# Kernel tuning notes

Hardware: AMD Instinct MI355X
Metric: run time of the kernel (lower is better)

The kernel has to match this reference:

```python
import jax, jax.numpy as jnp
from jax import lax
import numpy as np

DIM, HEADS, WIN = 192, 8, 8
B, H, W = 4, 256, 256


def setup_inputs() -> dict:
    key = jax.random.key(0)
    ks = jax.random.split(key, 4)
    s = 0.02
    return {
        "x": jax.random.normal(ks[0], (B, DIM, H, W), jnp.float32),
        "temperature": jnp.ones((HEADS, 1, 1), jnp.float32),
        "qkv_w": jax.random.normal(ks[1], (3 * DIM, DIM, 1, 1), jnp.float32) * s,
        "qkv_b": jnp.zeros((3 * DIM,), jnp.float32),
        "dw_w": jax.random.normal(ks[2], (3 * DIM, 1, 3, 3), jnp.float32) * s,
        "dw_b": jnp.zeros((3 * DIM,), jnp.float32),
        "proj_w": jax.random.normal(ks[3], (DIM, DIM, 1, 1), jnp.float32) * s,
        "proj_b": jnp.zeros((DIM,), jnp.float32),
    }


def _conv(x, w, b, groups=1, pad='VALID'):
    y = lax.conv_general_dilated(x, w, (1, 1), pad,
                                 feature_group_count=groups,
                                 dimension_numbers=('NCHW', 'OIHW', 'NCHW'))
    return y + b[None, :, None, None]


def _l2norm(x, eps=1e-12):
    # F.normalize(dim=-1): x / max(||x||_2, eps)
    n = jnp.sqrt(jnp.sum(x * x, axis=-1, keepdims=True))
    return x / jnp.maximum(n, eps)


def _chan_attn(q, k, v, temp):
    # q,k,v: [n, heads, c_per_head, d]; channel-wise (CxC) attention
    q = _l2norm(q)
    k = _l2norm(k)
    attn = jnp.einsum('nhcd,nhed->nhce', q, k) * temp[None]
    attn = jax.nn.softmax(attn, axis=-1)
    return jnp.einsum('nhce,nhed->nhcd', attn, v)


def reference(x, temperature, qkv_w, qkv_b, dw_w, dw_b, proj_w, proj_b):
    b, c, h, w = x.shape
    win, heads = WIN, HEADS
    cph = c // heads

    qkv = _conv(x, qkv_w, qkv_b)
    qkv = _conv(qkv, dw_w, dw_b, groups=3 * c, pad='SAME')  # depthwise 3x3
    q, k, v = jnp.split(qkv, 3, axis=1)

    # ---- local (windowed) branch ----
    def win_part(t):
        t = t.reshape(b, c, h // win, win, w // win, win)
        t = t.transpose(0, 2, 4, 1, 3, 5)
        return t.reshape(-1, heads, cph, win * win)

    o1 = _chan_attn(win_part(q), win_part(k), win_part(v), temperature)
    o1 = o1.reshape(b, h // win, w // win, c, win, win)
    o1 = o1.transpose(0, 3, 1, 4, 2, 5).reshape(b, c, h, w)

    # ---- global branch ----
    def flat(t):
        return t.reshape(b, heads, cph, h * w)

    o2 = _chan_attn(flat(q), flat(k), flat(v), temperature)
    o2 = o2.reshape(b, c, h, w)

    return _conv(o1 + o2, proj_w, proj_b)
```

## Files before the change

kernel.cpp:

```cpp
#include <hip/hip_runtime.h>
#include <hip/hip_bf16.h>
#include <cstdint>
#include <cstddef>

#define HWPIX 65536
#define IMGW 256
#define CDIM 192
#define C3 576
#define NBATCH 4
#define NHEADS 8
#define CPH 24
#define KP 104

using bf16 = __hip_bfloat16;
typedef __attribute__((ext_vector_type(8))) short short8;
typedef __attribute__((ext_vector_type(4))) float f32x4;
typedef unsigned int u32;
typedef unsigned short u16;

__device__ __forceinline__ float b2f(bf16 v) { return __bfloat162float(v); }
__device__ __forceinline__ bf16 f2b(float v) { return __float2bfloat16(v); }
__device__ __forceinline__ float bu2f(u16 h) { return __uint_as_float((u32)h << 16); }
__device__ __forceinline__ u16 f2bu(float x) {
    bf16 h = __float2bfloat16(x);
    return *reinterpret_cast<u16*>(&h);
}
__device__ __forceinline__ u32 pack2(float a, float b) {
    return (u32)f2bu(a) | ((u32)f2bu(b) << 16);
}

__global__ __launch_bounds__(256) void prep_weights(
    const float* __restrict__ W, u16* __restrict__ Wb, int n)
{
    int i = blockIdx.x * 256 + threadIdx.x;
    if (i < n) Wb[i] = f2bu(W[i]);
}

__global__ __launch_bounds__(256) void xprep_kernel(
    const float* __restrict__ X, u16* __restrict__ Xt)
{
    __shared__ float sX[CDIM * 68];
    const int b  = blockIdx.y;
    const int p0 = blockIdx.x * 64;
    const int tid = threadIdx.x;

#pragma unroll
    for (int i = 0; i < 12; ++i) {
        const int idx = tid + i * 256;
        const int p4 = idx & 15, k = idx >> 4;
        const float4 v = *reinterpret_cast<const float4*>(
            X + ((size_t)b * CDIM + k) * HWPIX + p0 + p4 * 4);
        *reinterpret_cast<float4*>(&sX[k * 68 + p4 * 4]) = v;
    }
    __syncthreads();

    const int p = tid >> 2;
    const int seg = tid & 3;
    u16* dst = Xt + ((size_t)b * HWPIX + p0 + p) * CDIM;
#pragma unroll
    for (int s = 0; s < 6; ++s) {
        const int blk = seg * 6 + s;
        float f[8];
#pragma unroll
        for (int j = 0; j < 8; ++j) f[j] = sX[(blk * 8 + j) * 68 + p];
        uint4 ov;
        ov.x = pack2(f[0], f[1]);
        ov.y = pack2(f[2], f[3]);
        ov.z = pack2(f[4], f[5]);
        ov.w = pack2(f[6], f[7]);
        *reinterpret_cast<uint4*>(dst + blk * 8) = ov;
    }
}

__global__ __launch_bounds__(256, 4) void conv_qkv_mfma(
    const u16* __restrict__ Xt, const u16* __restrict__ Wb,
    const float* __restrict__ bias, bf16* __restrict__ Y)
{
    __shared__ alignas(16) u16 sA[64 * KP];
    __shared__ alignas(16) u16 sB[128 * KP];
    __shared__ float sBias[64];

    int lin = blockIdx.x;
    lin = (lin & 7) * (18432 / 8) + (lin >> 3);
    const int co_t = lin % 9;
    const int rest = lin / 9;
    const int p_t = rest & 511;
    const int b   = rest >> 9;
    const int co0 = co_t * 64;
    const int p0  = p_t * 128;

    const int tid  = threadIdx.x;
    const int wave = tid >> 6;
    const int lane = tid & 63;
    const int r  = lane & 15;
    const int hk = lane >> 4;

    if (tid < 64) sBias[tid] = bias[co0 + tid];

    f32x4 acc[4][2];
#pragma unroll
    for (int i = 0; i < 4; ++i)
#pragma unroll
        for (int j = 0; j < 2; ++j) acc[i][j] = (f32x4){0.f, 0.f, 0.f, 0.f};

#pragma unroll
    for (int c = 0; c < 2; ++c) {
        {
            int idx = tid;
#pragma unroll
            for (int i = 0; i < 3; ++i, idx += 256) {
                const int row = idx / 12, cv = idx % 12;
                const uint4 v = *reinterpret_cast<const uint4*>(
                    Wb + (size_t)(co0 + row) * CDIM + c * 96 + cv * 8);
                *reinterpret_cast<uint4*>(&sA[row * KP + cv * 8]) = v;
            }
        }
        {
            int idx = tid;
#pragma unroll
            for (int i = 0; i < 6; ++i, idx += 256) {
                const int row = idx / 12, cv = idx % 12;
                const uint4 v = *reinterpret_cast<const uint4*>(
                    Xt + ((size_t)b * HWPIX + p0 + row) * CDIM + c * 96 + cv * 8);
                *reinterpret_cast<uint4*>(&sB[row * KP + cv * 8]) = v;
            }
        }
        __syncthreads();

#pragma unroll
        for (int ks = 0; ks < 3; ++ks) {
            const int kof = ks * 32 + hk * 8;
            const u16* pA = &sA[r * KP + kof];
            const u16* pB = &sB[(wave * 32 + r) * KP + kof];
            const short8 a0 = *reinterpret_cast<const short8*>(pA);
            const short8 a1 = *reinterpret_cast<const short8*>(pA + 16 * KP);
            const short8 a2 = *reinterpret_cast<const short8*>(pA + 32 * KP);
            const short8 a3 = *reinterpret_cast<const short8*>(pA + 48 * KP);
            const short8 b0 = *reinterpret_cast<const short8*>(pB);
            const short8 b1 = *reinterpret_cast<const short8*>(pB + 16 * KP);
            acc[0][0] = __builtin_amdgcn_mfma_f32_16x16x32_bf16(a0, b0, acc[0][0], 0, 0, 0);
            acc[1][0] = __builtin_amdgcn_mfma_f32_16x16x32_bf16(a1, b0, acc[1][0], 0, 0, 0);
            acc[2][0] = __builtin_amdgcn_mfma_f32_16x16x32_bf16(a2, b0, acc[2][0], 0, 0, 0);
            acc[3][0] = __builtin_amdgcn_mfma_f32_16x16x32_bf16(a3, b0, acc[3][0], 0, 0, 0);
            acc[0][1] = __builtin_amdgcn_mfma_f32_16x16x32_bf16(a0, b1, acc[0][1], 0, 0, 0);
            acc[1][1] = __builtin_amdgcn_mfma_f32_16x16x32_bf16(a1, b1, acc[1][1], 0, 0, 0);
            acc[2][1] = __builtin_amdgcn_mfma_f32_16x16x32_bf16(a2, b1, acc[2][1], 0, 0, 0);
            acc[3][1] = __builtin_amdgcn_mfma_f32_16x16x32_bf16(a3, b1, acc[3][1], 0, 0, 0);
        }
        __syncthreads();
    }

    u16* sOut = sB;
#pragma unroll
    for (int mf = 0; mf < 4; ++mf) {
#pragma unroll
        for (int j = 0; j < 4; ++j) {
            const int row = mf * 16 + hk * 4 + j;
            const float bs = sBias[row];
            sOut[row * 128 + wave * 32 + r]      = f2bu(acc[mf][0][j] + bs);
            sOut[row * 128 + wave * 32 + r + 16] = f2bu(acc[mf][1][j] + bs);
        }
    }
    __syncthreads();
#pragma unroll
    for (int i = 0; i < 4; ++i) {
        const int idx = tid + i * 256;
        const int row = idx >> 4, cq = idx & 15;
        const uint4 v = *reinterpret_cast<const uint4*>(&sOut[row * 128 + cq * 8]);
        *reinterpret_cast<uint4*>(
            &Y[((size_t)b * C3 + co0 + row) * HWPIX + p0 + cq * 8]) = v;
    }
}

__global__ __launch_bounds__(256, 4) void conv_proj_mfma(
    const u16* __restrict__ X, const u16* __restrict__ Wb,
    const float* __restrict__ bias, float* __restrict__ Y)
{
    __shared__ alignas(16) u16 sA[64 * KP];
    __shared__ alignas(16) u16 sB[128 * KP];
    __shared__ float sBias[64];

    int lin = blockIdx.x;
    lin = (lin & 7) * (6144 / 8) + (lin >> 3);
    const int co_t = lin % 3;
    const int rest = lin / 3;
    const int p_t = rest & 511;
    const int b   = rest >> 9;
    const int co0 = co_t * 64;
    const int p0  = p_t * 128;

    const int tid  = threadIdx.x;
    const int wave = tid >> 6;
    const int lane = tid & 63;
    const int r  = lane & 15;
    const int hk = lane >> 4;

    if (tid < 64) sBias[tid] = bias[co0 + tid];

    f32x4 acc[4][2];
#pragma unroll
    for (int i = 0; i < 4; ++i)
#pragma unroll
        for (int j = 0; j < 2; ++j) acc[i][j] = (f32x4){0.f, 0.f, 0.f, 0.f};

    const int p4 = tid & 31;
    const int kq = tid >> 5;

#pragma unroll
    for (int c = 0; c < 2; ++c) {
        {
            int idx = tid;
#pragma unroll
            for (int i = 0; i < 3; ++i, idx += 256) {
                const int row = idx / 12, cv = idx % 12;
                const uint4 v = *reinterpret_cast<const uint4*>(
                    Wb + (size_t)(co0 + row) * CDIM + c * 96 + cv * 8);
                *reinterpret_cast<uint4*>(&sA[row * KP + cv * 8]) = v;
            }
        }
        {
            const u16* Xc = X + ((size_t)b * CDIM + c * 96) * HWPIX + p0;
#pragma unroll
            for (int i = 0; i < 6; ++i) {
                const int kp = kq + i * 8;
                const int k  = kp * 2;
                const uint2 va = *reinterpret_cast<const uint2*>(
                    Xc + (size_t)k * HWPIX + p4 * 4);
                const uint2 vb = *reinterpret_cast<const uint2*>(
                    Xc + (size_t)(k + 1) * HWPIX + p4 * 4);
                const int col = (((kp >> 2) ^ (p4 & 3)) << 3) | (k & 7);
                const u32 w0 = (va.x & 0xffffu) | (vb.x << 16);
                const u32 w1 = (va.x >> 16)     | (vb.x & 0xffff0000u);
                const u32 w2 = (va.y & 0xffffu) | (vb.y << 16);
                const u32 w3 = (va.y >> 16)     | (vb.y & 0xffff0000u);
                const int rb = p4 * 4;
                *reinterpret_cast<u32*>(&sB[(rb    ) * KP + col]) = w0;
                *reinterpret_cast<u32*>(&sB[(rb + 1) * KP + col]) = w1;
                *reinterpret_cast<u32*>(&sB[(rb + 2) * KP + col]) = w2;
                *reinterpret_cast<u32*>(&sB[(rb + 3) * KP + col]) = w3;
            }
        }
        __syncthreads();

#pragma unroll
        for (int ks = 0; ks < 3; ++ks) {
            const int kof = ks * 32 + hk * 8;
            const u16* pA = &sA[r * KP + kof];
            const int rowb = wave * 32 + r;
            const int colr = (((kof >> 3) ^ ((rowb >> 2) & 3)) << 3);
            const u16* pB = &sB[rowb * KP + colr];
            const short8 a0 = *reinterpret_cast<const short8*>(pA);
            const short8 a1 = *reinterpret_cast<const short8*>(pA + 16 * KP);
            const short8 a2 = *reinterpret_cast<const short8*>(pA + 32 * KP);
            const short8 a3 = *reinterpret_cast<const short8*>(pA + 48 * KP);
            const short8 b0 = *reinterpret_cast<const short8*>(pB);
            const short8 b1 = *reinterpret_cast<const short8*>(pB + 16 * KP);
            acc[0][0] = __builtin_amdgcn_mfma_f32_16x16x32_bf16(a0, b0, acc[0][0], 0, 0, 0);
            acc[1][0] = __builtin_amdgcn_mfma_f32_16x16x32_bf16(a1, b0, acc[1][0], 0, 0, 0);
            acc[2][0] = __builtin_amdgcn_mfma_f32_16x16x32_bf16(a2, b0, acc[2][0], 0, 0, 0);
            acc[3][0] = __builtin_amdgcn_mfma_f32_16x16x32_bf16(a3, b0, acc[3][0], 0, 0, 0);
            acc[0][1] = __builtin_amdgcn_mfma_f32_16x16x32_bf16(a0, b1, acc[0][1], 0, 0, 0);
            acc[1][1] = __builtin_amdgcn_mfma_f32_16x16x32_bf16(a1, b1, acc[1][1], 0, 0, 0);
            acc[2][1] = __builtin_amdgcn_mfma_f32_16x16x32_bf16(a2, b1, acc[2][1], 0, 0, 0);
            acc[3][1] = __builtin_amdgcn_mfma_f32_16x16x32_bf16(a3, b1, acc[3][1], 0, 0, 0);
        }
        __syncthreads();
    }

#pragma unroll
    for (int mf = 0; mf < 4; ++mf) {
#pragma unroll
        for (int j = 0; j < 4; ++j) {
            const int co = co0 + mf * 16 + hk * 4 + j;
            const float bs = sBias[mf * 16 + hk * 4 + j];
            const size_t base = ((size_t)b * CDIM + co) * HWPIX + p0 + wave * 32 + r;
            Y[base]      = acc[mf][0][j] + bs;
            Y[base + 16] = acc[mf][1][j] + bs;
        }
    }
}

__global__ __launch_bounds__(256) void dwconv_kernel(
    const bf16* __restrict__ In, const float* __restrict__ Wd,
    const float* __restrict__ bd, bf16* __restrict__ Out)
{
    __shared__ alignas(16) u16 sIn[10 * 256];
    const int bc = blockIdx.y;
    const int c = bc % C3;
    const size_t base = (size_t)bc * HWPIX;
    const int r0 = blockIdx.x * 8;
    const int tid = threadIdx.x;

    for (int idx = tid; idx < 320; idx += 256) {
        const int lr = idx >> 5, ch = idx & 31;
        const int gr = r0 + lr - 1;
        uint4 v = {0u, 0u, 0u, 0u};
        if ((unsigned)gr < IMGW)
            v = *reinterpret_cast<const uint4*>(&In[base + (size_t)gr * IMGW + ch * 8]);
        *reinterpret_cast<uint4*>(&sIn[lr * 256 + ch * 8]) = v;
    }
    __syncthreads();

    float wg[9];
#pragma unroll
    for (int t = 0; t < 9; ++t) wg[t] = Wd[c * 9 + t];

    const int rr = tid >> 5;
    const int px0 = (tid & 31) * 8;
    const float bias = bd[c];
    float acc[8];
#pragma unroll
    for (int j = 0; j < 8; ++j) acc[j] = bias;

#pragma unroll
    for (int dy = 0; dy < 3; ++dy) {
        const int row = rr + dy;
        const u16* rp = &sIn[row * 256];
        const short8 mv = *reinterpret_cast<const short8*>(&rp[px0]);
        float m[8];
#pragma unroll
        for (int j = 0; j < 8; ++j) m[j] = bu2f((u16)mv[j]);
        const float lft = (px0 > 0) ? bu2f(rp[px0 - 1]) : 0.f;
        const float rgt = (px0 + 8 < 256) ? bu2f(rp[px0 + 8]) : 0.f;
        const float w0 = wg[dy * 3], w1 = wg[dy * 3 + 1], w2 = wg[dy * 3 + 2];

        acc[0] = fmaf(w0, lft, acc[0]);
        acc[0] = fmaf(w1, m[0], acc[0]);
        acc[0] = fmaf(w2, m[1], acc[0]);
#pragma unroll
        for (int j = 1; j < 7; ++j) {
            acc[j] = fmaf(w0, m[j - 1], acc[j]);
            acc[j] = fmaf(w1, m[j], acc[j]);
            acc[j] = fmaf(w2, m[j + 1], acc[j]);
        }
        acc[7] = fmaf(w0, m[6], acc[7]);
        acc[7] = fmaf(w1, m[7], acc[7]);
        acc[7] = fmaf(w2, rgt, acc[7]);
    }

    uint4 ov;
    ov.x = pack2(acc[0], acc[1]);
    ov.y = pack2(acc[2], acc[3]);
    ov.z = pack2(acc[4], acc[5]);
    ov.w = pack2(acc[6], acc[7]);
    *reinterpret_cast<uint4*>(&Out[base + (size_t)(r0 + rr) * IMGW + px0]) = ov;
}

#define CS 328
#define PS 40
#define OS 36

__global__ __launch_bounds__(256, 3) void local_attn_kernel(
    const bf16* __restrict__ QKV, const float* __restrict__ temp,
    const float* __restrict__ Ag, u16* __restrict__ Osum)
{
    __shared__ alignas(16) u16 sMem[3 * 24 * CS];
    __shared__ float snq[4 * 32], snk[4 * 32];
    __shared__ float sAg[576];
    u16* const sQ = sMem;
    u16* const sK = sMem + 24 * CS;
    u16* const sV = sMem + 48 * CS;
    u16* const sP = sQ;
    u16* const sO = sK;

    const int wy    = blockIdx.x >> 3;
    const int strip = blockIdx.x & 7;
    const int head  = blockIdx.y;
    const int b     = blockIdx.z;
    const int x0    = strip * 32;
    const int tid   = threadIdx.x;
    const int w     = tid >> 6;
    const int lane  = tid & 63;
    const int r     = lane & 15;
    const int hk    = lane >> 4;

    {
        const float* Asrc = Ag + ((size_t)(b * NHEADS + head)) * 576;
        for (int idx = tid; idx < 576; idx += 256) sAg[idx] = Asrc[idx];
    }

#pragma unroll
    for (int i = 0; i < 9; ++i) {
        const int idx = tid + i * 256;
        const int tensor = idx / 768;
        const int rem = idx - tensor * 768;
        const int c  = rem >> 5;
        const int rw = (rem >> 2) & 7;
        const int ch = rem & 3;
        const size_t g = ((size_t)b * C3 + tensor * CDIM + head * CPH + c) * HWPIX
                       + (size_t)(wy * 8 + rw) * IMGW + x0 + ch * 8;
        const uint4 v = *reinterpret_cast<const uint4*>(&QKV[g]);
        u16* dst = sMem + tensor * (24 * CS);
        *reinterpret_cast<uint4*>(&dst[c * CS + rw * 40 + ch * 8]) = v;
    }
    __syncthreads();

    if (tid < 192) {
        const int qk = tid / 96;
        const int rem = tid - qk * 96;
        const int ww = rem / 24, c = rem % 24;
        const u16* sT = qk ? sK : sQ;
        const int off = c * CS + ww * 8;
        float s = 0.f;
#pragma unroll
        for (int rw = 0; rw < 8; ++rw) {
            const int rw2 = (rw + c) & 7;
            const short8 v = *reinterpret_cast<const short8*>(&sT[off + rw2 * 40]);
#pragma unroll
            for (int j = 0; j < 8; ++j) {
                const float f = bu2f((u16)v[j]);
                s = fmaf(f, f, s);
            }
        }
        const float inv = 1.f / fmaxf(sqrtf(s), 1e-12f);
        if (qk) snk[ww * 32 + c] = inv; else snq[ww * 32 + c] = inv;
    }
    __syncthreads();

    f32x4 accg[2][2];
#pragma unroll
    for (int i = 0; i < 2; ++i)
#pragma unroll
        for (int j = 0; j < 2; ++j) accg[i][j] = (f32x4){0.f, 0.f, 0.f, 0.f};

#pragma unroll
    for (int kk = 0; kk < 2; ++kk) {
        const int colA = (kk * 4 + hk) * 40 + w * 8;
        const short8 aq0 = *reinterpret_cast<const short8*>(&sQ[(r     ) * CS + colA]);
        const short8 aq1 = *reinterpret_cast<const short8*>(&sQ[(16 + r) * CS + colA]);
        const short8 bk0 = *reinterpret_cast<const short8*>(&sK[(r     ) * CS + colA]);
        const short8 bk1 = *reinterpret_cast<const short8*>(&sK[(16 + r) * CS + colA]);
        accg[0][0] = __builtin_amdgcn_mfma_f32_16x16x32_bf16(aq0, bk0, accg[0][0], 0, 0, 0);
        accg[0][1] = __builtin_amdgcn_mfma_f32_16x16x32_bf16(aq0, bk1, accg[0][1], 0, 0, 0);
        accg[1][0] = __builtin_amdgcn_mfma_f32_16x16x32_bf16(aq1, bk0, accg[1][0], 0, 0, 0);
        accg[1][1] = __builtin_amdgcn_mfma_f32_16x16x32_bf16(aq1, bk1, accg[1][1], 0, 0, 0);
    }
    __syncthreads();

    const float t = temp[head];
    const int e0 = lane & 15;
    const bool v1 = e0 < 8;
    const float ink0 = snk[w * 32 + e0];
    const float ink1 = snk[w * 32 + 16 + e0];

#pragma unroll
    for (int ct = 0; ct < 2; ++ct) {
#pragma unroll
        for (int j = 0; j < 4; ++j) {
            const int cidx = ct * 16 + hk * 4 + j;
            const float inq = snq[w * 32 + (cidx < CPH ? cidx : 0)];
            const float g0 = accg[ct][0][j] * inq * ink0 * t;
            const float g1 = v1 ? accg[ct][1][j] * inq * ink1 * t : -1e30f;
            float m = fmaxf(g0, g1);
#pragma unroll
            for (int mk = 8; mk >= 1; mk >>= 1) m = fmaxf(m, __shfl_xor(m, mk));
            const float p0 = __expf(g0 - m);
            const float p1 = v1 ? __expf(g1 - m) : 0.f;
            float s = p0 + p1;
#pragma unroll
            for (int mk = 8; mk >= 1; mk >>= 1) s += __shfl_xor(s, mk);
            const float inv = 1.f / s;
            if (cidx < CPH) {
                sP[w * 32 * PS + cidx * PS + e0] = f2bu(p0 * inv + sAg[cidx * CPH + e0]);
                if (v1) sP[w * 32 * PS + cidx * PS + 16 + e0]
                    = f2bu(p1 * inv + sAg[cidx * CPH + 16 + e0]);
            }
        }
    }
    __syncthreads();

    f32x4 acco[2][4];
#pragma unroll
    for (int i = 0; i < 2; ++i)
#pragma unroll
        for (int j = 0; j < 4; ++j) acco[i][j] = (f32x4){0.f, 0.f, 0.f, 0.f};

    short8 afr[2];
#pragma unroll
    for (int ct = 0; ct < 2; ++ct) {
        if (hk < 3)
            afr[ct] = *reinterpret_cast<const short8*>(
                &sP[w * 32 * PS + (ct * 16 + r) * PS + hk * 8]);
        else
            afr[ct] = (short8){0, 0, 0, 0, 0, 0, 0, 0};
    }
#pragma unroll
    for (int nt = 0; nt < 4; ++nt) {
        const int px = nt * 16 + r;
        const int colV = (px >> 3) * 40 + w * 8 + (px & 7);
        short8 bfr;
        if (hk < 3) {
#pragma unroll
            for (int j = 0; j < 8; ++j)
                bfr[j] = (short)sV[(hk * 8 + j) * CS + colV];
        } else {
            bfr = (short8){0, 0, 0, 0, 0, 0, 0, 0};
        }
        acco[0][nt] = __builtin_amdgcn_mfma_f32_16x16x32_bf16(afr[0], bfr, acco[0][nt], 0, 0, 0);
        acco[1][nt] = __builtin_amdgcn_mfma_f32_16x16x32_bf16(afr[1], bfr, acco[1][nt], 0, 0, 0);
    }

#pragma unroll
    for (int ct = 0; ct < 2; ++ct) {
#pragma unroll
        for (int j = 0; j < 4; ++j) {
            const int cidx = ct * 16 + hk * 4 + j;
            if (cidx >= CPH) continue;
#pragma unroll
            for (int nt = 0; nt < 4; ++nt) {
                const int px = nt * 16 + r;
                const int rpx = px >> 3, pxl = px & 7;
                sO[(rpx * 24 + cidx) * OS + w * 8 + pxl] = f2bu(acco[ct][nt][j]);
            }
        }
    }
    __syncthreads();

#pragma unroll
    for (int i = 0; i < 3; ++i) {
        const int idx = tid + i * 256;
        const int q4 = idx & 3;
        const int row = idx >> 2;
        const int c = row % 24, rw = row / 24;
        const u16* src = &sO[row * OS + q4 * 8];
        const uint2 lo = *reinterpret_cast<const uint2*>(src);
        const uint2 hi = *reinterpret_cast<const uint2*>(src + 4);
        uint4 v = {lo.x, lo.y, hi.x, hi.y};
        *reinterpret_cast<uint4*>(
            &Osum[((size_t)b * CDIM + head * CPH + c) * HWPIX
                  + (size_t)(wy * 8 + rw) * IMGW + x0 + q4 * 8]) = v;
    }
}

#define GRS 520

__global__ __launch_bounds__(256) void gstats_kernel(
    const bf16* __restrict__ QKV, float* __restrict__ Gp)
{
    __shared__ alignas(16) u16 sq[32 * GRS];
    __shared__ alignas(16) u16 sk[32 * GRS];

    const int chunk = blockIdx.x;
    const int bh = blockIdx.y;
    const int b = bh >> 3, head = bh & 7;
    const int tid = threadIdx.x;
    const int w = tid >> 6, lane = tid & 63;
    const int r = lane & 15, hk = lane >> 4;

    const size_t qb = ((size_t)b * C3 + head * CPH) * HWPIX;
    const size_t kb = qb + (size_t)CDIM * HWPIX;

    for (int idx = tid; idx < 1040; idx += 256) {
        const int t = idx >= 520;
        const int o = idx - t * 520;
        u16* d = (t ? sk : sq) + 24 * GRS + o * 8;
        *reinterpret_cast<uint4*>(d) = (uint4){0u, 0u, 0u, 0u};
    }

    f32x4 acc[2][2];
#pragma unroll
    for (int i = 0; i < 2; ++i)
#pragma unroll
        for (int j = 0; j < 2; ++j) acc[i][j] = (f32x4){0.f, 0.f, 0.f, 0.f};
    float nacc = 0.f;
    const int nrow = tid >> 2;
    const int nq4  = tid & 3;

    for (int st = 0; st < 8; ++st) {
        const int d0 = chunk * 4096 + st * 512;
        __syncthreads();
#pragma unroll
        for (int i = 0; i < 12; ++i) {
            const int idx = tid + i * 256;
            const int t = idx >= 1536;
            const int rem = idx - t * 1536;
            const int c = rem >> 6, dv = rem & 63;
            const uint4 v = *reinterpret_cast<const uint4*>(
                &QKV[(t ? kb : qb) + (size_t)c * HWPIX + d0 + dv * 8]);
            u16* dst = (t ? sk : sq) + c * GRS + dv * 8;
            *reinterpret_cast<uint4*>(dst) = v;
        }
        __syncthreads();

#pragma unroll
        for (int ks = 0; ks < 4; ++ks) {
            const int kof = w * 128 + ks * 32 + hk * 8;
            const short8 aq0 = *reinterpret_cast<const short8*>(&sq[(r     ) * GRS + kof]);
            const short8 aq1 = *reinterpret_cast<const short8*>(&sq[(16 + r) * GRS + kof]);
            const short8 bk0 = *reinterpret_cast<const short8*>(&sk[(r     ) * GRS + kof]);
            const short8 bk1 = *reinterpret_cast<const short8*>(&sk[(16 + r) * GRS + kof]);
            acc[0][0] = __builtin_amdgcn_mfma_f32_16x16x32_bf16(aq0, bk0, acc[0][0], 0, 0, 0);
            acc[0][1] = __builtin_amdgcn_mfma_f32_16x16x32_bf16(aq0, bk1, acc[0][1], 0, 0, 0);
            acc[1][0] = __builtin_amdgcn_mfma_f32_16x16x32_bf16(aq1, bk0, acc[1][0], 0, 0, 0);
            acc[1][1] = __builtin_amdgcn_mfma_f32_16x16x32_bf16(aq1, bk1, acc[1][1], 0, 0, 0);
        }

        if (nrow < 48) {
            const u16* rp = (nrow < 24 ? &sq[nrow * GRS] : &sk[(nrow - 24) * GRS]) + nq4 * 128;
#pragma unroll
            for (int i = 0; i < 16; ++i) {
                const short8 v = *reinterpret_cast<const short8*>(&rp[i * 8]);
#pragma unroll
                for (int j = 0; j < 8; ++j) {
                    const float f = bu2f((u16)v[j]);
                    nacc = fmaf(f, f, nacc);
                }
            }
        }
    }
    __syncthreads();

    float* red = reinterpret_cast<float*>(sq);
#pragma unroll
    for (int ct = 0; ct < 2; ++ct) {
#pragma unroll
        for (int et = 0; et < 2; ++et) {
#pragma unroll
            for (int j = 0; j < 4; ++j) {
                const int c = ct * 16 + hk * 4 + j;
                const int e = et * 16 + r;
                if (c < CPH && e < CPH)
                    red[(w * 24 + c) * 25 + e] = acc[ct][et][j];
            }
        }
    }
    __syncthreads();

    float* dst = Gp + ((size_t)bh * 32 + chunk) * 624;
    for (int idx = tid; idx < 576; idx += 256) {
        const int c = idx / 24, e = idx % 24;
        const int o = c * 25 + e;
        dst[idx] = red[o] + red[600 + o] + red[1200 + o] + red[1800 + o];
    }

    float ns = nacc;
    ns += __shfl_xor(ns, 1);
    ns += __shfl_xor(ns, 2);
    if (nrow < 48 && nq4 == 0) {
        if (nrow < 24) dst[576 + nrow] = ns;
        else           dst[600 + (nrow - 24)] = ns;
    }
}

__global__ __launch_bounds__(64) void gsoftmax_kernel(
    const float* __restrict__ Gp, const float* __restrict__ temp,
    float* __restrict__ A)
{
    __shared__ float red[624];
    const int bh = blockIdx.x, head = bh & 7;
    const int tid = threadIdx.x;

    for (int jj = tid; jj < 624; jj += 64) {
        float s = 0.f;
        for (int ch = 0; ch < 16; ++ch) s += Gp[((size_t)bh * 32 + ch) * 624 + jj];
        red[jj] = s;
    }
    __syncthreads();

    if (tid < CPH) {
        const int c = tid;
        const float t = temp[head];
        const float inq = 1.f / fmaxf(sqrtf(red[576 + c]), 1e-12f);
        float l[CPH]; float m = -1e30f;
        for (int e = 0; e < CPH; ++e) {
            const float ink = 1.f / fmaxf(sqrtf(red[600 + e]), 1e-12f);
            l[e] = red[c * CPH + e] * inq * ink * t;
            m = fmaxf(m, l[e]);
        }
        float s = 0.f;
        for (int e = 0; e < CPH; ++e) { l[e] = expf(l[e] - m); s += l[e]; }
        const float inv = 1.f / s;
        for (int e = 0; e < CPH; ++e) A[(size_t)bh * 576 + c * CPH + e] = l[e] * inv;
    }
}

extern "C" void kernel_launch(void* const* d_in, const int* in_sizes, int n_in,
                              void* d_out, int out_size, void* d_ws, size_t ws_size,
                              hipStream_t stream) {
    const float* x           = (const float*)d_in[0];
    const float* temperature = (const float*)d_in[1];
    const float* qkv_w       = (const float*)d_in[2];
    const float* qkv_b       = (const float*)d_in[3];
    const float* dw_w        = (const float*)d_in[4];
    const float* dw_b        = (const float*)d_in[5];
    const float* proj_w      = (const float*)d_in[6];
    const float* proj_b      = (const float*)d_in[7];
    float* out = (float*)d_out;

    char* ws = (char*)d_ws;
    constexpr size_t QKV_ELEMS = (size_t)NBATCH * C3 * HWPIX;
    constexpr size_t QKV_BYTES = QKV_ELEMS * sizeof(bf16);

    bf16* qkv1 = (bf16*)ws;
    bf16* qkv2 = (bf16*)(ws + QKV_BYTES);
    u16*  osum = (u16*)ws;
    float* Gp   = (float*)(ws + 2 * QKV_BYTES);
    float* Amat = Gp + (size_t)32 * 32 * 624;
    u16*  Wb    = (u16*)Gp;
    u16*  Wpb   = (u16*)(Amat + 32 * 576);
    u16*  Xt    = (u16*)qkv2;

    prep_weights<<<(C3 * CDIM + 255) / 256, 256, 0, stream>>>(qkv_w, Wb, C3 * CDIM);
    prep_weights<<<(CDIM * CDIM + 255) / 256, 256, 0, stream>>>(proj_w, Wpb, CDIM * CDIM);

    xprep_kernel<<<dim3(HWPIX / 64, NBATCH), 256, 0, stream>>>(x, Xt);

    conv_qkv_mfma<<<9 * 512 * NBATCH, 256, 0, stream>>>(Xt, Wb, qkv_b, qkv1);

    dwconv_kernel<<<dim3(32, NBATCH * C3), 256, 0, stream>>>(
        qkv1, dw_w, dw_b, qkv2);

    gstats_kernel<<<dim3(16, 32), 256, 0, stream>>>(qkv2, Gp);

    gsoftmax_kernel<<<32, 64, 0, stream>>>(Gp, temperature, Amat);

    local_attn_kernel<<<dim3(256, NHEADS, NBATCH), 256, 0, stream>>>(
        qkv2, temperature, Amat, osum);

    conv_proj_mfma<<<3 * 512 * NBATCH, 256, 0, stream>>>(osum, Wpb, proj_b, out);
}
```

Before: 616.8 us.

## Use direct global-to-LDS loads with XOR swizzle in qkv conv; enlarge dwconv row tiles

Measured after the change: 629.1 us. No clear change (+2.0%).

```diff
diff --git a/kernel.cpp b/kernel.cpp
--- a/kernel.cpp
+++ b/kernel.cpp
@@ -11,6 +11,7 @@
 #define NHEADS 8
 #define CPH 24
 #define KP 104
+#define KQ 96
 
 using bf16 = __hip_bfloat16;
 typedef __attribute__((ext_vector_type(8))) short short8;
@@ -27,6 +28,11 @@
 }
 __device__ __forceinline__ u32 pack2(float a, float b) {
     return (u32)f2bu(a) | ((u32)f2bu(b) << 16);
+}
+__device__ __forceinline__ void gload_lds16(const u16* gsrc, u16* ldst) {
+    __builtin_amdgcn_global_load_lds(
+        (const __attribute__((address_space(1))) void*)gsrc,
+        (__attribute__((address_space(3))) void*)ldst, 16, 0, 0);
 }
 
 __global__ __launch_bounds__(256) void prep_weights(
@@ -76,8 +82,7 @@
     const u16* __restrict__ Xt, const u16* __restrict__ Wb,
     const float* __restrict__ bias, bf16* __restrict__ Y)
 {
-    __shared__ alignas(16) u16 sA[64 * KP];
-    __shared__ alignas(16) u16 sB[128 * KP];
+    __shared__ alignas(16) u16 sAB[192 * KQ];
     __shared__ float sBias[64];
 
     int lin = blockIdx.x;
@@ -106,38 +111,35 @@
 #pragma unroll
     for (int c = 0; c < 2; ++c) {
         {
-            int idx = tid;
-#pragma unroll
-            for (int i = 0; i < 3; ++i, idx += 256) {
-                const int row = idx / 12, cv = idx % 12;
-                const uint4 v = *reinterpret_cast<const uint4*>(
-                    Wb + (size_t)(co0 + row) * CDIM + c * 96 + cv * 8);
-                *reinterpret_cast<uint4*>(&sA[row * KP + cv * 8]) = v;
-            }
-        }
-        {
-            int idx = tid;
-#pragma unroll
-            for (int i = 0; i < 6; ++i, idx += 256) {
-                const int row = idx / 12, cv = idx % 12;
-                const uint4 v = *reinterpret_cast<const uint4*>(
-                    Xt + ((size_t)b * HWPIX + p0 + row) * CDIM + c * 96 + cv * 8);
-                *reinterpret_cast<uint4*>(&sB[row * KP + cv * 8]) = v;
+            u16* wbase = sAB + wave * 4608;
+#pragma unroll
+            for (int i = 0; i < 9; ++i) {
+                const int m  = i * 64 + lane;
+                const int gr = wave * 48 + m / 12;
+                const int blk = m % 12;
+                const int sblk = blk ^ ((gr >> 2) & 3);
+                const u16* gsrc = (gr < 64)
+                    ? (Wb + (size_t)(co0 + gr) * CDIM)
+                    : (Xt + ((size_t)b * HWPIX + p0 + gr - 64) * CDIM);
+                gload_lds16(gsrc + c * 96 + sblk * 8, wbase + i * 512);
             }
         }
         __syncthreads();
 
 #pragma unroll
         for (int ks = 0; ks < 3; ++ks) {
-            const int kof = ks * 32 + hk * 8;
-            const u16* pA = &sA[r * KP + kof];
-            const u16* pB = &sB[(wave * 32 + r) * KP + kof];
+            const int kb = ks * 4 + hk;
+            const int fA = (r >> 2) & 3;
+            const u16* pA = &sAB[r * KQ + (kb ^ fA) * 8];
+            const int rowb = 64 + wave * 32 + r;
+            const int fB = (rowb >> 2) & 3;
+            const u16* pB = &sAB[rowb * KQ + (kb ^ fB) * 8];
             const short8 a0 = *reinterpret_cast<const short8*>(pA);
-            const short8 a1 = *reinterpret_cast<const short8*>(pA + 16 * KP);
-            const short8 a2 = *reinterpret_cast<const short8*>(pA + 32 * KP);
-            const short8 a3 = *reinterpret_cast<const short8*>(pA + 48 * KP);
+            const short8 a1 = *reinterpret_cast<const short8*>(pA + 16 * KQ);
+            const short8 a2 = *reinterpret_cast<const short8*>(pA + 32 * KQ);
+            const short8 a3 = *reinterpret_cast<const short8*>(pA + 48 * KQ);
             const short8 b0 = *reinterpret_cast<const short8*>(pB);
-            const short8 b1 = *reinterpret_cast<const short8*>(pB + 16 * KP);
+            const short8 b1 = *reinterpret_cast<const short8*>(pB + 16 * KQ);
             acc[0][0] = __builtin_amdgcn_mfma_f32_16x16x32_bf16(a0, b0, acc[0][0], 0, 0, 0);
             acc[1][0] = __builtin_amdgcn_mfma_f32_16x16x32_bf16(a1, b0, acc[1][0], 0, 0, 0);
             acc[2][0] = __builtin_amdgcn_mfma_f32_16x16x32_bf16(a2, b0, acc[2][0], 0, 0, 0);
@@ -150,15 +152,16 @@
         __syncthreads();
     }
 
-    u16* sOut = sB;
+#define OS2 132
+    u16* sOut = sAB;
 #pragma unroll
     for (int mf = 0; mf < 4; ++mf) {
 #pragma unroll
         for (int j = 0; j < 4; ++j) {
             const int row = mf * 16 + hk * 4 + j;
             const float bs = sBias[row];
-            sOut[row * 128 + wave * 32 + r]      = f2bu(acc[mf][0][j] + bs);
-            sOut[row * 128 + wave * 32 + r + 16] = f2bu(acc[mf][1][j] + bs);
+            sOut[row * OS2 + wave * 32 + r]      = f2bu(acc[mf][0][j] + bs);
+            sOut[row * OS2 + wave * 32 + r + 16] = f2bu(acc[mf][1][j] + bs);
         }
     }
     __syncthreads();
@@ -166,7 +169,10 @@
     for (int i = 0; i < 4; ++i) {
         const int idx = tid + i * 256;
         const int row = idx >> 4, cq = idx & 15;
-        const uint4 v = *reinterpret_cast<const uint4*>(&sOut[row * 128 + cq * 8]);
+        const u16* src = &sOut[row * OS2 + cq * 8];
+        const uint2 lo = *reinterpret_cast<const uint2*>(src);
+        const uint2 hi = *reinterpret_cast<const uint2*>(src + 4);
+        uint4 v = {lo.x, lo.y, hi.x, hi.y};
         *reinterpret_cast<uint4*>(
             &Y[((size_t)b * C3 + co0 + row) * HWPIX + p0 + cq * 8]) = v;
     }
@@ -284,14 +290,14 @@
     const bf16* __restrict__ In, const float* __restrict__ Wd,
     const float* __restrict__ bd, bf16* __restrict__ Out)
 {
-    __shared__ alignas(16) u16 sIn[10 * 256];
+    __shared__ alignas(16) u16 sIn[34 * 256];
     const int bc = blockIdx.y;
     const int c = bc % C3;
     const size_t base = (size_t)bc * HWPIX;
-    const int r0 = blockIdx.x * 8;
+    const int r0 = blockIdx.x * 32;
     const int tid = threadIdx.x;
 
-    for (int idx = tid; idx < 320; idx += 256) {
+    for (int idx = tid; idx < 34 * 32; idx += 256) {
         const int lr = idx >> 5, ch = idx & 31;
         const int gr = r0 + lr - 1;
         uint4 v = {0u, 0u, 0u, 0u};
@@ -305,45 +311,49 @@
 #pragma unroll
     for (int t = 0; t < 9; ++t) wg[t] = Wd[c * 9 + t];
 
-    const int rr = tid >> 5;
+    const int rr  = tid >> 5;
     const int px0 = (tid & 31) * 8;
     const float bias = bd[c];
-    float acc[8];
-#pragma unroll
-    for (int j = 0; j < 8; ++j) acc[j] = bias;
-
-#pragma unroll
-    for (int dy = 0; dy < 3; ++dy) {
-        const int row = rr + dy;
-        const u16* rp = &sIn[row * 256];
-        const short8 mv = *reinterpret_cast<const short8*>(&rp[px0]);
-        float m[8];
-#pragma unroll
-        for (int j = 0; j < 8; ++j) m[j] = bu2f((u16)mv[j]);
-        const float lft = (px0 > 0) ? bu2f(rp[px0 - 1]) : 0.f;
-        const float rgt = (px0 + 8 < 256) ? bu2f(rp[px0 + 8]) : 0.f;
-        const float w0 = wg[dy * 3], w1 = wg[dy * 3 + 1], w2 = wg[dy * 3 + 2];
-
-        acc[0] = fmaf(w0, lft, acc[0]);
-        acc[0] = fmaf(w1, m[0], acc[0]);
-        acc[0] = fmaf(w2, m[1], acc[0]);
-#pragma unroll
-        for (int j = 1; j < 7; ++j) {
-            acc[j] = fmaf(w0, m[j - 1], acc[j]);
-            acc[j] = fmaf(w1, m[j], acc[j]);
-            acc[j] = fmaf(w2, m[j + 1], acc[j]);
-        }
-        acc[7] = fmaf(w0, m[6], acc[7]);
-        acc[7] = fmaf(w1, m[7], acc[7]);
-        acc[7] = fmaf(w2, rgt, acc[7]);
-    }
-
-    uint4 ov;
-    ov.x = pack2(acc[0], acc[1]);
-    ov.y = pack2(acc[2], acc[3]);
-    ov.z = pack2(acc[4], acc[5]);
-    ov.w = pack2(acc[6], acc[7]);
-    *reinterpret_cast<uint4*>(&Out[base + (size_t)(r0 + rr) * IMGW + px0]) = ov;
+
+#pragma unroll
+    for (int kk = 0; kk < 4; ++kk) {
+        const int orow = rr + kk * 8;
+        float acc[8];
+#pragma unroll
+        for (int j = 0; j < 8; ++j) acc[j] = bias;
+
+#pragma unroll
+        for (int dy = 0; dy < 3; ++dy) {
+            const u16* rp = &sIn[(orow + dy) * 256];
+            const short8 mv = *reinterpret_cast<const short8*>(&rp[px0]);
+            float m[8];
+#pragma unroll
+            for (int j = 0; j < 8; ++j) m[j] = bu2f((u16)mv[j]);
+            const float lft = (px0 > 0) ? bu2f(rp[px0 - 1]) : 0.f;
+            const float rgt = (px0 + 8 < 256) ? bu2f(rp[px0 + 8]) : 0.f;
+            const float w0 = wg[dy * 3], w1 = wg[dy * 3 + 1], w2 = wg[dy * 3 + 2];
+
+            acc[0] = fmaf(w0, lft, acc[0]);
+            acc[0] = fmaf(w1, m[0], acc[0]);
+            acc[0] = fmaf(w2, m[1], acc[0]);
+#pragma unroll
+            for (int j = 1; j < 7; ++j) {
+                acc[j] = fmaf(w0, m[j - 1], acc[j]);
+                acc[j] = fmaf(w1, m[j], acc[j]);
+                acc[j] = fmaf(w2, m[j + 1], acc[j]);
+            }
+            acc[7] = fmaf(w0, m[6], acc[7]);
+            acc[7] = fmaf(w1, m[7], acc[7]);
+            acc[7] = fmaf(w2, rgt, acc[7]);
+        }
+
+        uint4 ov;
+        ov.x = pack2(acc[0], acc[1]);
+        ov.y = pack2(acc[2], acc[3]);
+        ov.z = pack2(acc[4], acc[5]);
+        ov.w = pack2(acc[6], acc[7]);
+        *reinterpret_cast<uint4*>(&Out[base + (size_t)(r0 + orow) * IMGW + px0]) = ov;
+    }
 }
 
 #define CS 328
@@ -707,7 +717,7 @@
 
     conv_qkv_mfma<<<9 * 512 * NBATCH, 256, 0, stream>>>(Xt, Wb, qkv_b, qkv1);
 
-    dwconv_kernel<<<dim3(32, NBATCH * C3), 256, 0, stream>>>(
+    dwconv_kernel<<<dim3(8, NBATCH * C3), 256, 0, stream>>>(
         qkv1, dw_w, dw_b, qkv2);
 
     gstats_kernel<<<dim3(16, 32), 256, 0, stream>>>(qkv2, Gp);
```
